# Optimization experiments

Measured on AMD Instinct MI355X. Metric: run time of the kernel, lower is better.

Reference implementation:

```python
import jax, jax.numpy as jnp
import numpy as np

N = 100000   # nodes
E = 1000000  # edges
IN = 64      # in_dim
H = 4        # hidden heads
D = 32       # num_hidden (per-head dim)
C = 32       # num_classes
NEG_SLOPE = 0.2


def setup_inputs() -> dict:
    key = jax.random.key(0)
    ks = jax.random.split(key, 9)
    def init(k, shape, fan):
        return jax.random.normal(k, shape, jnp.float32) * np.float32(1.0 / np.sqrt(fan))
    return {
        "T": jax.random.normal(ks[0], (N, IN), jnp.float32),
        "src": jax.random.randint(ks[1], (E,), 0, N),
        "dst": jax.random.randint(ks[2], (E,), 0, N),
        "W0": init(ks[3], (IN, H * D), IN),
        "al0": init(ks[4], (H, D), D),
        "ar0": init(ks[5], (H, D), D),
        "W1": init(ks[6], (H * D, C), H * D),
        "al1": init(ks[7], (1, C), C),
        "ar1": init(ks[8], (1, C), C),
    }


def _gat_layer(x, W, al, ar, src, dst, heads, dim):
    # DGL GATConv: linear proj -> per-edge additive attention -> edge softmax
    # (segment softmax over incoming edges of each dst node) -> weighted sum.
    h = (x @ W).reshape(N, heads, dim)                      # [N,H,D]
    el = (h * al[None]).sum(-1)                             # [N,H]
    er = (h * ar[None]).sum(-1)                             # [N,H]
    e = jax.nn.leaky_relu(el[src] + er[dst], NEG_SLOPE)     # [E,H]
    m = jax.ops.segment_max(e, dst, num_segments=N)         # [N,H]
    ex = jnp.exp(e - m[dst])                                # [E,H]
    ssum = jax.ops.segment_sum(ex, dst, num_segments=N)     # [N,H]
    alpha = ex / ssum[dst]                                  # [E,H]
    msg = h[src] * alpha[:, :, None]                        # [E,H,D]
    return jax.ops.segment_sum(msg, dst, num_segments=N)    # [N,H,D]


def reference(T, src, dst, W0, al0, ar0, W1, al1, ar1):
    # hidden GAT layer: concat heads + elu
    h = _gat_layer(T, W0, al0, ar0, src, dst, H, D)
    h = jax.nn.elu(h).reshape(N, H * D)
    # output GAT layer: 1 head, mean over heads, no activation
    out = _gat_layer(h, W1, al1, ar1, src, dst, 1, C).mean(axis=1)  # [N,C]
    # AvgPooling over the single graph -> [1,C]
    return out.mean(axis=0, keepdims=True)
```

## Files before the change

### kernel.cpp

```cpp
#include <hip/hip_runtime.h>
#include <math.h>

#define NN 100000
#define NE 1000000
#define CAP 32
#define BSH 8
#define BNODES 256
#define NBUK 391
#define BUKCAP 6144
#define EPB 4096
#define ABLK 245

constexpr size_t AL(size_t x){ return (x + 255) & ~size_t(255); }
constexpr size_t OFF_H0  = 0;
constexpr size_t OFF_H1P = OFF_H0  + AL(size_t(NN)*32*4);
constexpr size_t OFF_EL0 = OFF_H1P + AL(size_t(NN)*8*4);
constexpr size_t OFF_ER0 = OFF_EL0 + AL(size_t(NN)*4*4);
constexpr size_t OFF_EL1 = OFF_ER0 + AL(size_t(NN)*4*4);
constexpr size_t OFF_ER1 = OFF_EL1 + AL(size_t(NN)*4);
constexpr size_t OFF_CNT = OFF_ER1 + AL(size_t(NN)*4);
constexpr size_t OFF_CSRF= OFF_CNT + AL(size_t(NN)*4);
constexpr size_t OFF_BUK = OFF_CSRF+ AL(size_t(NN)*CAP*4);
constexpr size_t OFF_BUKC= OFF_BUK + AL(size_t(NBUK)*BUKCAP*4);
constexpr size_t OFF_P2  = OFF_BUKC+ AL(size_t(NBUK)*4);
constexpr size_t OFF_PART= OFF_P2  + AL(25*32*4);

using f32x2 = __attribute__((ext_vector_type(2))) float;
using f16x2 = __attribute__((ext_vector_type(2))) _Float16;
using half8 = __attribute__((ext_vector_type(8))) _Float16;
using f32x4v = __attribute__((ext_vector_type(4))) float;

__device__ __forceinline__ float lrelu(float x){ return x >= 0.f ? x : 0.2f*x; }
__device__ __forceinline__ unsigned pkf16(float a, float b){
  f16x2 h; h.x = (_Float16)a; h.y = (_Float16)b;
  return __builtin_bit_cast(unsigned, h);
}
__device__ __forceinline__ f16x2 u2h(unsigned u){ return __builtin_bit_cast(f16x2, u); }

__device__ __forceinline__ void fp8fma(uint2 u, float x, float* acc){
  f32x2 a0 = __builtin_amdgcn_cvt_pk_f32_fp8((int)u.x, false);
  f32x2 a1 = __builtin_amdgcn_cvt_pk_f32_fp8((int)u.x, true);
  f32x2 a2 = __builtin_amdgcn_cvt_pk_f32_fp8((int)u.y, false);
  f32x2 a3 = __builtin_amdgcn_cvt_pk_f32_fp8((int)u.y, true);
  acc[0] = fmaf(x, a0.x, acc[0]); acc[1] = fmaf(x, a0.y, acc[1]);
  acc[2] = fmaf(x, a1.x, acc[2]); acc[3] = fmaf(x, a1.y, acc[3]);
  acc[4] = fmaf(x, a2.x, acc[4]); acc[5] = fmaf(x, a2.y, acc[5]);
  acc[6] = fmaf(x, a3.x, acc[6]); acc[7] = fmaf(x, a3.y, acc[7]);
}

__global__ __launch_bounds__(256) void k_gemm1(const float* __restrict__ T,
    const float* __restrict__ W0, const float* __restrict__ al0, const float* __restrict__ ar0,
    unsigned* __restrict__ h0p, float* __restrict__ el0, float* __restrict__ er0,
    int* __restrict__ bukCnt){
  __shared__ float w[64*128];
  __shared__ float tr[64][65];
  int t = threadIdx.x;
  int base = blockIdx.x * 64;
  if (blockIdx.x == 0){
    for (int i = t; i < NBUK; i += 256) bukCnt[i] = 0;
  }
  {
    const float4* W4 = (const float4*)W0;
    float4* w4 = (float4*)w;
    #pragma unroll
    for (int i = 0; i < 8; ++i) w4[t + 256*i] = W4[t + 256*i];
  }
  for (int i = t; i < 1024; i += 256){
    int rr = i >> 4, f = i & 15;
    int n = base + rr;
    float4 v = make_float4(0.f,0.f,0.f,0.f);
    if (n < NN) v = ((const float4*)(T + (size_t)n*64))[f];
    int kc = f << 2;
    tr[rr][kc] = v.x; tr[rr][kc+1] = v.y; tr[rr][kc+2] = v.z; tr[rr][kc+3] = v.w;
  }
  __syncthreads();
  int tx = t & 15, ty = t >> 4;
  int r0 = ty * 4;
  int jA = tx * 4, jB = 64 + tx * 4;
  float accA[4][4], accB[4][4];
  #pragma unroll
  for (int rr = 0; rr < 4; ++rr)
    #pragma unroll
    for (int j = 0; j < 4; ++j){ accA[rr][j] = 0.f; accB[rr][j] = 0.f; }
  #pragma unroll 2
  for (int k = 0; k < 64; ++k){
    float4 wA = *(const float4*)&w[k*128 + jA];
    float4 wB = *(const float4*)&w[k*128 + jB];
    #pragma unroll
    for (int rr = 0; rr < 4; ++rr){
      float a = tr[r0 + rr][k];
      accA[rr][0] = fmaf(a, wA.x, accA[rr][0]);
      accA[rr][1] = fmaf(a, wA.y, accA[rr][1]);
      accA[rr][2] = fmaf(a, wA.z, accA[rr][2]);
      accA[rr][3] = fmaf(a, wA.w, accA[rr][3]);
      accB[rr][0] = fmaf(a, wB.x, accB[rr][0]);
      accB[rr][1] = fmaf(a, wB.y, accB[rr][1]);
      accB[rr][2] = fmaf(a, wB.z, accB[rr][2]);
      accB[rr][3] = fmaf(a, wB.w, accB[rr][3]);
    }
  }
  float alA[4], arA[4], alB[4], arB[4];
  #pragma unroll
  for (int j = 0; j < 4; ++j){
    alA[j] = al0[jA+j]; arA[j] = ar0[jA+j];
    alB[j] = al0[jB+j]; arB[j] = ar0[jB+j];
  }
  #pragma unroll
  for (int rr = 0; rr < 4; ++rr){
    int n = base + r0 + rr;
    float vlA=0.f, vrA=0.f, vlB=0.f, vrB=0.f;
    #pragma unroll
    for (int j = 0; j < 4; ++j){
      vlA = fmaf(accA[rr][j], alA[j], vlA);
      vrA = fmaf(accA[rr][j], arA[j], vrA);
      vlB = fmaf(accB[rr][j], alB[j], vlB);
      vrB = fmaf(accB[rr][j], arB[j], vrB);
    }
    int pa = __builtin_amdgcn_cvt_pk_fp8_f32(accA[rr][0], accA[rr][1], 0, false);
    pa     = __builtin_amdgcn_cvt_pk_fp8_f32(accA[rr][2], accA[rr][3], pa, true);
    int pb = __builtin_amdgcn_cvt_pk_fp8_f32(accB[rr][0], accB[rr][1], 0, false);
    pb     = __builtin_amdgcn_cvt_pk_fp8_f32(accB[rr][2], accB[rr][3], pb, true);
    #pragma unroll
    for (int m = 1; m <= 4; m <<= 1){
      vlA += __shfl_xor(vlA, m); vrA += __shfl_xor(vrA, m);
      vlB += __shfl_xor(vlB, m); vrB += __shfl_xor(vrB, m);
    }
    if (n < NN){
      h0p[(size_t)n*32 + tx]      = (unsigned)pa;
      h0p[(size_t)n*32 + 16 + tx] = (unsigned)pb;
      if (tx == 0){
        el0[n*4 + 0] = vlA; er0[n*4 + 0] = vrA;
        el0[n*4 + 2] = vlB; er0[n*4 + 2] = vrB;
      } else if (tx == 8){
        el0[n*4 + 1] = vlA; er0[n*4 + 1] = vrA;
        el0[n*4 + 3] = vlB; er0[n*4 + 3] = vrB;
      }
    }
  }
}

__global__ __launch_bounds__(256) void k_bucket(const int* __restrict__ src,
    const int* __restrict__ dst, int* __restrict__ bukCnt, unsigned* __restrict__ buk){
  __shared__ int hist[NBUK];
  __shared__ int base[NBUK];
  int t = threadIdx.x;
  int e0 = blockIdx.x * EPB;
  int ecnt = min(EPB, NE - e0);
  int myd[16], mys[16];
  for (int i = t; i < NBUK; i += 256) hist[i] = 0;
  __syncthreads();
  #pragma unroll
  for (int q = 0; q < 16; ++q){
    int i = t + q*256;
    if (i < ecnt){
      myd[q] = dst[e0 + i];
      mys[q] = src[e0 + i];
      atomicAdd(&hist[myd[q] >> BSH], 1);
    }
  }
  __syncthreads();
  for (int i = t; i < NBUK; i += 256){
    int c = hist[i];
    base[i] = c ? atomicAdd(&bukCnt[i], (c + 15) & ~15) : 0;
  }
  __syncthreads();
  for (int i = t; i < NBUK; i += 256) hist[i] = 0;
  __syncthreads();
  #pragma unroll
  for (int q = 0; q < 16; ++q){
    int i = t + q*256;
    if (i < ecnt){
      int b = myd[q] >> BSH;
      int pos = base[b] + atomicAdd(&hist[b], 1);
      if (pos < BUKCAP)
        buk[(size_t)b * BUKCAP + pos] = ((unsigned)mys[q] << BSH) | (unsigned)(myd[q] & (BNODES-1));
    }
  }
  __syncthreads();
  for (int i = t; i < NBUK; i += 256){
    int c = hist[i];
    if (c){
      int p0 = base[i] + c;
      int p1 = base[i] + ((c + 15) & ~15);
      for (int p = p0; p < p1; ++p)
        if (p < BUKCAP) buk[(size_t)i * BUKCAP + p] = 0xFFFFFFFFu;
    }
  }
}

__global__ __launch_bounds__(256) void k_csr(const unsigned* __restrict__ buk,
    const int* __restrict__ bukCnt, int* __restrict__ cnt, int* __restrict__ csrF){
  __shared__ int lcnt[BNODES];
  __shared__ int lcsr[BNODES*CAP];
  int t = threadIdx.x;
  int b = blockIdx.x;
  int nbase = b << BSH;
  for (int i = t; i < BNODES; i += 256) lcnt[i] = 0;
  __syncthreads();
  int ecnt = min(bukCnt[b], BUKCAP);
  for (int i = t; i < ecnt; i += 256){
    unsigned v = buk[(size_t)b * BUKCAP + i];
    if (v == 0xFFFFFFFFu) continue;
    int dloc = v & (BNODES-1);
    int slot = atomicAdd(&lcnt[dloc], 1);
    if (slot < CAP) lcsr[(dloc << 5) + slot] = (int)(v >> BSH);
  }
  __syncthreads();
  for (int i = t; i < BNODES; i += 256){
    int n = nbase + i;
    if (n < NN) cnt[n] = min(lcnt[i], CAP);
  }
  const int4* l4 = (const int4*)lcsr;
  int4* g4 = (int4*)csrF;
  for (int k = t; k < BNODES*(CAP/4); k += 256){
    int nloc = k >> 3, q = k & 7;
    int n = nbase + nloc;
    if (n < NN && q*4 < lcnt[nloc]) g4[((size_t)n << 3) + q] = l4[k];
  }
}

__global__ __launch_bounds__(256) void k_agg0g2(const unsigned* __restrict__ h0p,
    const float* __restrict__ el0, const float* __restrict__ er0,
    const int* __restrict__ cnt, const int* __restrict__ csrF,
    const float* __restrict__ W1, const float* __restrict__ al1, const float* __restrict__ ar1,
    unsigned* __restrict__ h1f, float* __restrict__ el1, float* __restrict__ er1){
  __shared__ unsigned wcm[32*68];
  __shared__ int   idxs[4][4][33];
  __shared__ float exv [4][4][33][4];
  __shared__ float elw[2][2][16];
  int t = threadIdx.x;
  for (int i = t; i < 2048; i += 256){
    int c = i & 31, kw = i >> 5;
    wcm[c*68 + kw] = pkf16(W1[(2*kw)*32 + c], W1[(2*kw+1)*32 + c]);
  }
  int wib = t >> 6, lane = t & 63;
  int g = lane >> 4, l4 = lane & 15;
  int nbase = blockIdx.x * 16;
  int n = nbase + wib*4 + g;
  int deg = min(cnt[n], CAP);
  const float4* el4p = (const float4*)el0;
  float4 er4 = ((const float4*)er0)[n];
  for (int e = l4; e < deg; e += 16){
    int sj = csrF[(n << 5) + e];
    float4 e4 = el4p[sj];
    float4 x;
    x.x = __expf(lrelu(e4.x + er4.x));
    x.y = __expf(lrelu(e4.y + er4.y));
    x.z = __expf(lrelu(e4.z + er4.z));
    x.w = __expf(lrelu(e4.w + er4.w));
    idxs[wib][g][e] = sj;
    *(float4*)&exv[wib][g][e][0] = x;
  }
  __builtin_amdgcn_wave_barrier();
  int head = l4 >> 2;
  float acc[8];
  #pragma unroll
  for (int i = 0; i < 8; ++i) acc[i] = 0.f;
  float ssum = 0.f;
  int j = 0;
  for (; j + 3 < deg; j += 4){
    int s0 = idxs[wib][g][j],   s1 = idxs[wib][g][j+1];
    int s2 = idxs[wib][g][j+2], s3 = idxs[wib][g][j+3];
    float x0 = exv[wib][g][j][head],   x1 = exv[wib][g][j+1][head];
    float x2 = exv[wib][g][j+2][head], x3 = exv[wib][g][j+3][head];
    uint2 u0 = *(const uint2*)&h0p[(size_t)s0*32 + l4*2];
    uint2 u1 = *(const uint2*)&h0p[(size_t)s1*32 + l4*2];
    uint2 u2 = *(const uint2*)&h0p[(size_t)s2*32 + l4*2];
    uint2 u3 = *(const uint2*)&h0p[(size_t)s3*32 + l4*2];
    fp8fma(u0, x0, acc); fp8fma(u1, x1, acc);
    fp8fma(u2, x2, acc); fp8fma(u3, x3, acc);
    ssum += x0 + x1 + x2 + x3;
  }
  for (; j < deg; ++j){
    int sa = idxs[wib][g][j];
    float xa = exv[wib][g][j][head];
    uint2 ua = *(const uint2*)&h0p[(size_t)sa*32 + l4*2];
    fp8fma(ua, xa, acc);
    ssum += xa;
  }
  __builtin_amdgcn_wave_barrier();
  float inv = (deg > 0) ? 1.f / ssum : 0.f;
  float o[8];
  #pragma unroll
  for (int i = 0; i < 8; ++i){
    float v = acc[i] * inv;
    o[i] = v > 0.f ? v : expm1f(v);
  }
  uint4 up;
  up.x = pkf16(o[0], o[1]);
  up.y = pkf16(o[2], o[3]);
  up.z = pkf16(o[4], o[5]);
  up.w = pkf16(o[6], o[7]);
  unsigned* hrowBase = (unsigned*)&exv[wib][0][0][0];
  *(uint4*)(hrowBase + g*68 + l4*4) = up;
  __syncthreads();
  if (wib < 2){
    int w = wib;
    int q = lane >> 4, c = lane & 15;
    const unsigned* hb = (const unsigned*)exv;
    int aoff = (c >> 2)*528 + (c & 3)*68 + q*4;
    const unsigned* bb = &wcm[(w*16 + c)*68];
    f32x4v acc4 = {0.f, 0.f, 0.f, 0.f};
    #pragma unroll
    for (int kk = 0; kk < 4; ++kk){
      uint4 av = *(const uint4*)(hb + aoff + kk*16);
      uint4 bv = *(const uint4*)(bb + kk*16 + q*4);
      acc4 = __builtin_amdgcn_mfma_f32_16x16x32_f16(
          __builtin_bit_cast(half8, av), __builtin_bit_cast(half8, bv), acc4, 0, 0, 0);
    }
    float al_c = al1[w*16 + c], ar_c = ar1[w*16 + c];
    #pragma unroll
    for (int i = 0; i < 4; ++i){
      float vl = acc4[i] * al_c, vr = acc4[i] * ar_c;
      #pragma unroll
      for (int m = 1; m <= 8; m <<= 1){ vl += __shfl_xor(vl, m); vr += __shfl_xor(vr, m); }
      if (c == 0){ elw[w][0][q*4 + i] = vl; elw[w][1][q*4 + i] = vr; }
    }
    unsigned myw[4];
    #pragma unroll
    for (int i = 0; i < 4; ++i){
      float nb1 = __shfl_xor(acc4[i], 1);
      int pk = __builtin_amdgcn_cvt_pk_fp8_f32(acc4[i], nb1, 0, false) & 0xFFFF;
      int pk2 = __shfl_xor(pk, 2);
      myw[i] = (unsigned)(pk | (pk2 << 16));
    }
    if ((c & 3) == 0){
      #pragma unroll
      for (int i = 0; i < 4; ++i)
        h1f[(size_t)(nbase + q*4 + i)*8 + w*4 + (c >> 2)] = myw[i];
    }
  }
  __syncthreads();
  if (t < 16){
    el1[nbase + t] = elw[0][0][t] + elw[1][0][t];
    er1[nbase + t] = elw[0][1][t] + elw[1][1][t];
  }
}

__global__ __launch_bounds__(256) void k_agg1(const unsigned* __restrict__ h1f,
    const float* __restrict__ el1, const float* __restrict__ er1,
    const int* __restrict__ cnt, const int* __restrict__ csrF, float* __restrict__ part){
  __shared__ int   idxs[4][4][33];
  __shared__ float exs [4][4][33];
  __shared__ float sp[4][32];
  int t = threadIdx.x;
  int wib = t >> 6, lane = t & 63;
  int g = lane >> 4, l4 = lane & 15;
  int n = blockIdx.x*16 + wib*4 + g;
  int deg = min(cnt[n], CAP);
  float ern = er1[n];
  for (int e = l4; e < deg; e += 16){
    int sj = csrF[(n << 5) + e];
    idxs[wib][g][e] = sj;
    exs[wib][g][e] = __expf(lrelu(el1[sj] + ern));
  }
  __builtin_amdgcn_wave_barrier();
  int word = l4 >> 1;
  bool hiSel = (l4 & 1);
  float a0 = 0.f, a1 = 0.f, ssum = 0.f;
  int j = 0;
  for (; j + 3 < deg; j += 4){
    int s0 = idxs[wib][g][j],   s1 = idxs[wib][g][j+1];
    int s2 = idxs[wib][g][j+2], s3 = idxs[wib][g][j+3];
    float x0 = exs[wib][g][j],   x1 = exs[wib][g][j+1];
    float x2 = exs[wib][g][j+2], x3 = exs[wib][g][j+3];
    unsigned u0 = h1f[(size_t)s0*8 + word];
    unsigned u1 = h1f[(size_t)s1*8 + word];
    unsigned u2 = h1f[(size_t)s2*8 + word];
    unsigned u3 = h1f[(size_t)s3*8 + word];
    f32x2 lo, hi; float px, py;
    lo = __builtin_amdgcn_cvt_pk_f32_fp8((int)u0, false);
    hi = __builtin_amdgcn_cvt_pk_f32_fp8((int)u0, true);
    px = hiSel ? hi.x : lo.x; py = hiSel ? hi.y : lo.y;
    a0 = fmaf(x0, px, a0); a1 = fmaf(x0, py, a1);
    lo = __builtin_amdgcn_cvt_pk_f32_fp8((int)u1, false);
    hi = __builtin_amdgcn_cvt_pk_f32_fp8((int)u1, true);
    px = hiSel ? hi.x : lo.x; py = hiSel ? hi.y : lo.y;
    a0 = fmaf(x1, px, a0); a1 = fmaf(x1, py, a1);
    lo = __builtin_amdgcn_cvt_pk_f32_fp8((int)u2, false);
    hi = __builtin_amdgcn_cvt_pk_f32_fp8((int)u2, true);
    px = hiSel ? hi.x : lo.x; py = hiSel ? hi.y : lo.y;
    a0 = fmaf(x2, px, a0); a1 = fmaf(x2, py, a1);
    lo = __builtin_amdgcn_cvt_pk_f32_fp8((int)u3, false);
    hi = __builtin_amdgcn_cvt_pk_f32_fp8((int)u3, true);
    px = hiSel ? hi.x : lo.x; py = hiSel ? hi.y : lo.y;
    a0 = fmaf(x3, px, a0); a1 = fmaf(x3, py, a1);
    ssum += x0 + x1 + x2 + x3;
  }
  for (; j < deg; ++j){
    int sa = idxs[wib][g][j];
    float xa = exs[wib][g][j];
    unsigned ua = h1f[(size_t)sa*8 + word];
    f32x2 lo = __builtin_amdgcn_cvt_pk_f32_fp8((int)ua, false);
    f32x2 hi = __builtin_amdgcn_cvt_pk_f32_fp8((int)ua, true);
    float px = hiSel ? hi.x : lo.x, py = hiSel ? hi.y : lo.y;
    a0 = fmaf(xa, px, a0); a1 = fmaf(xa, py, a1);
    ssum += xa;
  }
  float inv = (deg > 0) ? 1.f / ssum : 0.f;
  a0 *= inv; a1 *= inv;
  a0 += __shfl_xor(a0, 16); a0 += __shfl_xor(a0, 32);
  a1 += __shfl_xor(a1, 16); a1 += __shfl_xor(a1, 32);
  if (lane < 16){ sp[wib][2*l4] = a0; sp[wib][2*l4+1] = a1; }
  __syncthreads();
  if (t < 32){
    part[(size_t)blockIdx.x*32 + t] = sp[0][t] + sp[1][t] + sp[2][t] + sp[3][t];
  }
}

__global__ __launch_bounds__(256) void k_red(const float* __restrict__ part, float* __restrict__ part2){
  __shared__ float red[8][32];
  int t = threadIdx.x;
  int c = t & 31, g = t >> 5;
  size_t base = (size_t)blockIdx.x * 250;
  float s = 0.f;
  for (int r = g; r < 250; r += 8) s += part[(base + r)*32 + c];
  red[g][c] = s;
  __syncthreads();
  if (t < 32){
    float tot = 0.f;
    #pragma unroll
    for (int g2 = 0; g2 < 8; ++g2) tot += red[g2][t];
    part2[(size_t)blockIdx.x*32 + t] = tot;
  }
}

__global__ void k_final(const float* __restrict__ part2, float* __restrict__ out){
  int c = threadIdx.x;
  if (c < 32){
    float s = 0.f;
    #pragma unroll
    for (int r = 0; r < 25; ++r) s += part2[r*32 + c];
    out[c] = s * (1.f / NN);
  }
}

extern "C" void kernel_launch(void* const* d_in, const int* in_sizes, int n_in,
                              void* d_out, int out_size, void* d_ws, size_t ws_size,
                              hipStream_t stream) {
  (void)in_sizes; (void)n_in; (void)out_size; (void)ws_size;
  const float* T   = (const float*)d_in[0];
  const int*  srcI = (const int*)d_in[1];
  const int*  dstI = (const int*)d_in[2];
  const float* W0  = (const float*)d_in[3];
  const float* al0 = (const float*)d_in[4];
  const float* ar0 = (const float*)d_in[5];
  const float* W1  = (const float*)d_in[6];
  const float* al1 = (const float*)d_in[7];
  const float* ar1 = (const float*)d_in[8];

  char* ws = (char*)d_ws;
  unsigned* h0p  = (unsigned*)(ws + OFF_H0);
  unsigned* h1f  = (unsigned*)(ws + OFF_H1P);
  float* el0  = (float*)(ws + OFF_EL0);
  float* er0  = (float*)(ws + OFF_ER0);
  float* el1  = (float*)(ws + OFF_EL1);
  float* er1  = (float*)(ws + OFF_ER1);
  int*   cnt  = (int*)(ws + OFF_CNT);
  int*   csrF = (int*)(ws + OFF_CSRF);
  unsigned* buk = (unsigned*)(ws + OFF_BUK);
  int*   bukCnt = (int*)(ws + OFF_BUKC);
  float* part2 = (float*)(ws + OFF_P2);
  float* part = (float*)(ws + OFF_PART);
  float* out  = (float*)d_out;

  const int NB_G  = 1563;
  const int NB_A  = NN / 16;

  k_gemm1  <<<NB_G, 256, 0, stream>>>(T, W0, al0, ar0, h0p, el0, er0, bukCnt);
  k_bucket <<<ABLK, 256, 0, stream>>>(srcI, dstI, bukCnt, buk);
  k_csr    <<<NBUK, 256, 0, stream>>>(buk, bukCnt, cnt, csrF);
  k_agg0g2 <<<NB_A, 256, 0, stream>>>(h0p, el0, er0, cnt, csrF,
                                      W1, al1, ar1, h1f, el1, er1);
  k_agg1   <<<NB_A, 256, 0, stream>>>(h1f, el1, er1, cnt, csrF, part);
  k_red    <<<25, 256, 0, stream>>>(part, part2);
  k_final  <<<1, 64, 0, stream>>>(part2, out);
}
```

Measured before the change: 131.4 us.

## Fuse edge bucketing into GEMM kernel with per-block cells, merge reductions

The edge-bucketing pass is folded into the first GEMM kernel as extra blocks, so both run in one launch and overlap. Each block now writes to its own fixed-width cell per bucket, which removes the global atomic reservation and the padding writes. k_csr scatters directly to global CSR instead of staging in shared memory, and the two final reduction kernels are merged into one 1024-thread kernel. The trade-offs are that cells overflowing 48 edges silently drop edges, the CSR pass now walks cells serially per thread with scattered global writes, and the single-block final reduction has less parallelism.

```diff
diff --git a/kernel.cpp b/kernel.cpp
--- a/kernel.cpp
+++ b/kernel.cpp
@@ -7,9 +7,10 @@
 #define BSH 8
 #define BNODES 256
 #define NBUK 391
-#define BUKCAP 6144
+#define CELLW 48
 #define EPB 4096
 #define ABLK 245
+#define NB_G 1563
 
 constexpr size_t AL(size_t x){ return (x + 255) & ~size_t(255); }
 constexpr size_t OFF_H0  = 0;
@@ -21,9 +22,8 @@
 constexpr size_t OFF_CNT = OFF_ER1 + AL(size_t(NN)*4);
 constexpr size_t OFF_CSRF= OFF_CNT + AL(size_t(NN)*4);
 constexpr size_t OFF_BUK = OFF_CSRF+ AL(size_t(NN)*CAP*4);
-constexpr size_t OFF_BUKC= OFF_BUK + AL(size_t(NBUK)*BUKCAP*4);
-constexpr size_t OFF_P2  = OFF_BUKC+ AL(size_t(NBUK)*4);
-constexpr size_t OFF_PART= OFF_P2  + AL(25*32*4);
+constexpr size_t OFF_CNT2= OFF_BUK + AL(size_t(NBUK)*ABLK*CELLW*4);
+constexpr size_t OFF_PART= OFF_CNT2+ AL(size_t(ABLK)*NBUK*4);
 
 using f32x2 = __attribute__((ext_vector_type(2))) float;
 using f16x2 = __attribute__((ext_vector_type(2))) _Float16;
@@ -35,7 +35,6 @@
   f16x2 h; h.x = (_Float16)a; h.y = (_Float16)b;
   return __builtin_bit_cast(unsigned, h);
 }
-__device__ __forceinline__ f16x2 u2h(unsigned u){ return __builtin_bit_cast(f16x2, u); }
 
 __device__ __forceinline__ void fp8fma(uint2 u, float x, float* acc){
   f32x2 a0 = __builtin_amdgcn_cvt_pk_f32_fp8((int)u.x, false);
@@ -48,17 +47,34 @@
   acc[6] = fmaf(x, a3.x, acc[6]); acc[7] = fmaf(x, a3.y, acc[7]);
 }
 
-__global__ __launch_bounds__(256) void k_gemm1(const float* __restrict__ T,
+__global__ __launch_bounds__(256) void k_g1b(const float* __restrict__ T,
     const float* __restrict__ W0, const float* __restrict__ al0, const float* __restrict__ ar0,
     unsigned* __restrict__ h0p, float* __restrict__ el0, float* __restrict__ er0,
-    int* __restrict__ bukCnt){
+    const int* __restrict__ src, const int* __restrict__ dst,
+    unsigned* __restrict__ buk, int* __restrict__ cnt2){
   __shared__ float w[64*128];
   __shared__ float tr[64][65];
   int t = threadIdx.x;
-  int base = blockIdx.x * 64;
-  if (blockIdx.x == 0){
-    for (int i = t; i < NBUK; i += 256) bukCnt[i] = 0;
-  }
+  if (blockIdx.x < ABLK){
+    int* hist = (int*)w;
+    int blk = blockIdx.x;
+    int e0 = blk * EPB;
+    int ecnt = min(EPB, NE - e0);
+    for (int i = t; i < NBUK; i += 256) hist[i] = 0;
+    __syncthreads();
+    for (int i = t; i < ecnt; i += 256){
+      int d = dst[e0 + i];
+      int s = src[e0 + i];
+      int b = d >> BSH;
+      int pos = atomicAdd(&hist[b], 1);
+      if (pos < CELLW)
+        buk[((size_t)b*ABLK + blk)*CELLW + pos] = ((unsigned)s << BSH) | (unsigned)(d & (BNODES-1));
+    }
+    __syncthreads();
+    for (int i = t; i < NBUK; i += 256) cnt2[(size_t)blk*NBUK + i] = hist[i];
+    return;
+  }
+  int base = (blockIdx.x - ABLK) * 64;
   {
     const float4* W4 = (const float4*)W0;
     float4* w4 = (float4*)w;
@@ -139,83 +155,28 @@
   }
 }
 
-__global__ __launch_bounds__(256) void k_bucket(const int* __restrict__ src,
-    const int* __restrict__ dst, int* __restrict__ bukCnt, unsigned* __restrict__ buk){
-  __shared__ int hist[NBUK];
-  __shared__ int base[NBUK];
-  int t = threadIdx.x;
-  int e0 = blockIdx.x * EPB;
-  int ecnt = min(EPB, NE - e0);
-  int myd[16], mys[16];
-  for (int i = t; i < NBUK; i += 256) hist[i] = 0;
-  __syncthreads();
-  #pragma unroll
-  for (int q = 0; q < 16; ++q){
-    int i = t + q*256;
-    if (i < ecnt){
-      myd[q] = dst[e0 + i];
-      mys[q] = src[e0 + i];
-      atomicAdd(&hist[myd[q] >> BSH], 1);
-    }
-  }
-  __syncthreads();
-  for (int i = t; i < NBUK; i += 256){
-    int c = hist[i];
-    base[i] = c ? atomicAdd(&bukCnt[i], (c + 15) & ~15) : 0;
-  }
-  __syncthreads();
-  for (int i = t; i < NBUK; i += 256) hist[i] = 0;
-  __syncthreads();
-  #pragma unroll
-  for (int q = 0; q < 16; ++q){
-    int i = t + q*256;
-    if (i < ecnt){
-      int b = myd[q] >> BSH;
-      int pos = base[b] + atomicAdd(&hist[b], 1);
-      if (pos < BUKCAP)
-        buk[(size_t)b * BUKCAP + pos] = ((unsigned)mys[q] << BSH) | (unsigned)(myd[q] & (BNODES-1));
-    }
-  }
-  __syncthreads();
-  for (int i = t; i < NBUK; i += 256){
-    int c = hist[i];
-    if (c){
-      int p0 = base[i] + c;
-      int p1 = base[i] + ((c + 15) & ~15);
-      for (int p = p0; p < p1; ++p)
-        if (p < BUKCAP) buk[(size_t)i * BUKCAP + p] = 0xFFFFFFFFu;
-    }
-  }
-}
-
 __global__ __launch_bounds__(256) void k_csr(const unsigned* __restrict__ buk,
-    const int* __restrict__ bukCnt, int* __restrict__ cnt, int* __restrict__ csrF){
+    const int* __restrict__ cnt2, int* __restrict__ cnt, int* __restrict__ csrF){
   __shared__ int lcnt[BNODES];
-  __shared__ int lcsr[BNODES*CAP];
   int t = threadIdx.x;
   int b = blockIdx.x;
   int nbase = b << BSH;
   for (int i = t; i < BNODES; i += 256) lcnt[i] = 0;
   __syncthreads();
-  int ecnt = min(bukCnt[b], BUKCAP);
-  for (int i = t; i < ecnt; i += 256){
-    unsigned v = buk[(size_t)b * BUKCAP + i];
-    if (v == 0xFFFFFFFFu) continue;
-    int dloc = v & (BNODES-1);
-    int slot = atomicAdd(&lcnt[dloc], 1);
-    if (slot < CAP) lcsr[(dloc << 5) + slot] = (int)(v >> BSH);
+  for (int cell = t; cell < ABLK; cell += 256){
+    int c2 = min(cnt2[(size_t)cell*NBUK + b], CELLW);
+    const unsigned* cp = &buk[((size_t)b*ABLK + cell)*CELLW];
+    for (int i = 0; i < c2; ++i){
+      unsigned v = cp[i];
+      int dloc = v & (BNODES-1);
+      int slot = atomicAdd(&lcnt[dloc], 1);
+      if (slot < CAP) csrF[((size_t)(nbase + dloc) << 5) + slot] = (int)(v >> BSH);
+    }
   }
   __syncthreads();
   for (int i = t; i < BNODES; i += 256){
     int n = nbase + i;
     if (n < NN) cnt[n] = min(lcnt[i], CAP);
-  }
-  const int4* l4 = (const int4*)lcsr;
-  int4* g4 = (int4*)csrF;
-  for (int k = t; k < BNODES*(CAP/4); k += 256){
-    int nloc = k >> 3, q = k & 7;
-    int n = nbase + nloc;
-    if (n < NN && q*4 < lcnt[nloc]) g4[((size_t)n << 3) + q] = l4[k];
   }
 }
 
@@ -408,30 +369,19 @@
   }
 }
 
-__global__ __launch_bounds__(256) void k_red(const float* __restrict__ part, float* __restrict__ part2){
-  __shared__ float red[8][32];
+__global__ __launch_bounds__(1024) void k_redfin(const float* __restrict__ part, float* __restrict__ out){
+  __shared__ float red[32][32];
   int t = threadIdx.x;
   int c = t & 31, g = t >> 5;
-  size_t base = (size_t)blockIdx.x * 250;
   float s = 0.f;
-  for (int r = g; r < 250; r += 8) s += part[(base + r)*32 + c];
+  for (int r = g; r < 6250; r += 32) s += part[(size_t)r*32 + c];
   red[g][c] = s;
   __syncthreads();
   if (t < 32){
     float tot = 0.f;
     #pragma unroll
-    for (int g2 = 0; g2 < 8; ++g2) tot += red[g2][t];
-    part2[(size_t)blockIdx.x*32 + t] = tot;
-  }
-}
-
-__global__ void k_final(const float* __restrict__ part2, float* __restrict__ out){
-  int c = threadIdx.x;
-  if (c < 32){
-    float s = 0.f;
-    #pragma unroll
-    for (int r = 0; r < 25; ++r) s += part2[r*32 + c];
-    out[c] = s * (1.f / NN);
+    for (int g2 = 0; g2 < 32; ++g2) tot += red[g2][t];
+    out[t] = tot * (1.f / NN);
   }
 }
 
@@ -459,20 +409,17 @@
   int*   cnt  = (int*)(ws + OFF_CNT);
   int*   csrF = (int*)(ws + OFF_CSRF);
   unsigned* buk = (unsigned*)(ws + OFF_BUK);
-  int*   bukCnt = (int*)(ws + OFF_BUKC);
-  float* part2 = (float*)(ws + OFF_P2);
+  int*   cnt2 = (int*)(ws + OFF_CNT2);
   float* part = (float*)(ws + OFF_PART);
   float* out  = (float*)d_out;
 
-  const int NB_G  = 1563;
   const int NB_A  = NN / 16;
 
-  k_gemm1  <<<NB_G, 256, 0, stream>>>(T, W0, al0, ar0, h0p, el0, er0, bukCnt);
-  k_bucket <<<ABLK, 256, 0, stream>>>(srcI, dstI, bukCnt, buk);
-  k_csr    <<<NBUK, 256, 0, stream>>>(buk, bukCnt, cnt, csrF);
+  k_g1b    <<<ABLK + NB_G, 256, 0, stream>>>(T, W0, al0, ar0, h0p, el0, er0,
+                                             srcI, dstI, buk, cnt2);
+  k_csr    <<<NBUK, 256, 0, stream>>>(buk, cnt2, cnt, csrF);
   k_agg0g2 <<<NB_A, 256, 0, stream>>>(h0p, el0, er0, cnt, csrF,
                                       W1, al1, ar1, h1f, el1, er1);
   k_agg1   <<<NB_A, 256, 0, stream>>>(h1f, el1, er1, cnt, csrF, part);
-  k_red    <<<25, 256, 0, stream>>>(part, part2);
-  k_final  <<<1, 64, 0, stream>>>(part2, out);
-}
+  k_redfin <<<1, 1024, 0, stream>>>(part, out);
+}
```

New measurement: 160.3 us. +22.0%, slower.
